# Optimization experiments

Measured on AMD Instinct MI355X. Metric: run time of the kernel, lower is better.

## Reference

```python
import jax, jax.numpy as jnp
import numpy as np
import math

B, T, C = 4, 2048, 1024
H = 16
DH = C // H
SCALE = 1.0 / math.sqrt(DH)


def setup_inputs() -> dict:
    key = jax.random.key(0)
    k1, k2, k3 = jax.random.split(key, 3)
    x = jax.random.normal(k1, (B, T, C), dtype=jnp.float32)
    # init_unit_norm: randn / sqrt(d_in)
    W_qkv = jax.random.normal(k2, (3 * C, C), dtype=jnp.float32) / math.sqrt(C)
    W_out = jax.random.normal(k3, (C, C), dtype=jnp.float32) / math.sqrt(C)
    return {"x": x, "W_qkv": W_qkv, "W_out": W_out}


def reference(x, W_qkv, W_out):
    b, t, c = x.shape
    qkv = x @ W_qkv.T                      # [B,T,3C]
    q, k, v = jnp.split(qkv, 3, axis=-1)
    # [B,T,C] -> [B,H,T,Dh]
    q = q.reshape(b, t, H, DH).transpose(0, 2, 1, 3)
    k = k.reshape(b, t, H, DH).transpose(0, 2, 1, 3)
    v = v.reshape(b, t, H, DH).transpose(0, 2, 1, 3)
    scores = jnp.einsum('bhtd,bhsd->bhts', q, k) * SCALE  # [B,H,T,T]
    mask = jnp.tril(jnp.ones((t, t), dtype=bool))
    scores = jnp.where(mask, scores, 0.0)  # no softmax
    attn = jnp.einsum('bhts,bhsd->bhtd', scores, v)       # [B,H,T,Dh]
    attn = attn.transpose(0, 2, 1, 3).reshape(b, t, c)
    return attn @ W_out.T
```

## Files before the change

### kernel.cpp

```cpp
#include <hip/hip_runtime.h>

#define TT 2048
#define CC 1024

typedef __attribute__((ext_vector_type(8))) __bf16 bf16x8;
typedef __attribute__((ext_vector_type(4))) float f32x4;
typedef unsigned int u32;

__device__ __forceinline__ short f2bf(float f) {
  u32 u = __float_as_uint(f);
  u += 0x7fffu + ((u >> 16) & 1u);
  return (short)(u >> 16);
}

#if __has_builtin(__builtin_amdgcn_cvt_pk_bf16_f32)
__device__ __forceinline__ u32 pack2(float a, float b) {
  auto v = __builtin_amdgcn_cvt_pk_bf16_f32(a, b);
  return __builtin_bit_cast(u32, v);
}
#else
__device__ __forceinline__ u32 pack2(float a, float b) {
  u32 ua = __float_as_uint(a), ub = __float_as_uint(b);
  ua += 0x7fffu + ((ua >> 16) & 1u);
  ub += 0x7fffu + ((ub >> 16) & 1u);
  return (ua >> 16) | (ub & 0xffff0000u);
}
#endif

__global__ void cvt_bf16(const float* __restrict__ in, short* __restrict__ out, int n4) {
  int i = blockIdx.x * blockDim.x + threadIdx.x;
  if (i >= n4) return;
  float4 f = reinterpret_cast<const float4*>(in)[i];
  short4 s;
  s.x = f2bf(f.x); s.y = f2bf(f.y); s.z = f2bf(f.z); s.w = f2bf(f.w);
  reinterpret_cast<short4*>(out)[i] = s;
}

__global__ void cvt_wqkv(const float* __restrict__ in, short* __restrict__ out, int n4) {
  int i = blockIdx.x * blockDim.x + threadIdx.x;
  if (i >= n4) return;
  float sc = (i * 4 < 1048576) ? 0.125f : 1.0f;
  float4 f = reinterpret_cast<const float4*>(in)[i];
  short4 s;
  s.x = f2bf(f.x * sc); s.y = f2bf(f.y * sc); s.z = f2bf(f.z * sc); s.w = f2bf(f.w * sc);
  reinterpret_cast<short4*>(out)[i] = s;
}

__device__ __forceinline__ void storev(float* p, float v) { *p = v; }
__device__ __forceinline__ void storev(short* p, float v) { *p = f2bf(v); }

#if __has_builtin(__builtin_amdgcn_global_load_lds)
#define HAVE_GLD_LDS 1
__device__ __forceinline__ void gld_lds16(const short* g, short* l) {
  __builtin_amdgcn_global_load_lds((const __attribute__((address_space(1))) u32*)g,
                                   (__attribute__((address_space(3))) u32*)l, 16, 0, 0);
}
#endif

template <typename OutT>
__global__ __launch_bounds__(256) void gemm_bt(const short* __restrict__ A,
                                               const short* __restrict__ B,
                                               OutT* __restrict__ Cm,
                                               int M, int N, int K) {
  __shared__ __align__(16) short As[128 * 32];
  __shared__ __align__(16) short Bs[128 * 32];
  const int tid = threadIdx.x;
  const int wave = tid >> 6, lane = tid & 63;
  const int quad = lane >> 4, nl = lane & 15;
  const int m0 = blockIdx.x * 128, n0 = blockIdx.y * 128;
  const int wr = (wave >> 1) * 64, wc = (wave & 1) * 64;
  f32x4 acc[4][4] = {};
  for (int k0 = 0; k0 < K; k0 += 32) {
    __syncthreads();
#pragma unroll
    for (int i = 0; i < 2; ++i) {
      int idx = tid + i * 256;
      int row = idx >> 2, cg = idx & 3;
#if HAVE_GLD_LDS
      gld_lds16(&A[(size_t)(m0 + row) * K + k0 + cg * 8], &As[(i * 256 + wave * 64) * 8]);
      gld_lds16(&B[(size_t)(n0 + row) * K + k0 + cg * 8], &Bs[(i * 256 + wave * 64) * 8]);
#else
      *reinterpret_cast<uint4*>(&As[row * 32 + cg * 8]) =
          *reinterpret_cast<const uint4*>(&A[(size_t)(m0 + row) * K + k0 + cg * 8]);
      *reinterpret_cast<uint4*>(&Bs[row * 32 + cg * 8]) =
          *reinterpret_cast<const uint4*>(&B[(size_t)(n0 + row) * K + k0 + cg * 8]);
#endif
    }
    __syncthreads();
    bf16x8 af[4], bfr[4];
#pragma unroll
    for (int i = 0; i < 4; ++i)
      af[i] = *reinterpret_cast<const bf16x8*>(&As[(wr + i * 16 + nl) * 32 + quad * 8]);
#pragma unroll
    for (int i = 0; i < 4; ++i)
      bfr[i] = *reinterpret_cast<const bf16x8*>(&Bs[(wc + i * 16 + nl) * 32 + quad * 8]);
#pragma unroll
    for (int mi = 0; mi < 4; ++mi)
#pragma unroll
      for (int ni = 0; ni < 4; ++ni)
        acc[mi][ni] = __builtin_amdgcn_mfma_f32_16x16x32_bf16(af[mi], bfr[ni], acc[mi][ni], 0, 0, 0);
  }
#pragma unroll
  for (int mi = 0; mi < 4; ++mi)
#pragma unroll
    for (int ni = 0; ni < 4; ++ni) {
      int row = m0 + wr + mi * 16 + quad * 4;
      int col = n0 + wc + ni * 16 + nl;
#pragma unroll
      for (int r = 0; r < 4; ++r)
        storev(&Cm[(size_t)(row + r) * N + col], acc[mi][ni][r]);
    }
}

__global__ __launch_bounds__(256) void transpose_v(const short* __restrict__ qkv,
                                                   short* __restrict__ vt) {
  __shared__ short Ls[64 * 68];
  const int bh = blockIdx.y, tb = blockIdx.x;
  const int b = bh >> 4, h = bh & 15;
  const int tid = threadIdx.x;
  const short* src = qkv + (size_t)(b * TT + tb * 64) * (3 * CC) + 2 * CC + h * 64;
#pragma unroll
  for (int i = 0; i < 2; ++i) {
    int idx = tid + i * 256;
    int tl = idx >> 3, dc = idx & 7;
    uint4 d4 = *reinterpret_cast<const uint4*>(&src[(size_t)tl * (3 * CC) + dc * 8]);
    *reinterpret_cast<uint2*>(&Ls[tl * 68 + dc * 8]) = make_uint2(d4.x, d4.y);
    *reinterpret_cast<uint2*>(&Ls[tl * 68 + dc * 8 + 4]) = make_uint2(d4.z, d4.w);
  }
  __syncthreads();
  short* dst = vt + (size_t)(bh * 64) * TT + tb * 64;
#pragma unroll
  for (int i = 0; i < 2; ++i) {
    int idx = tid + i * 256;
    int dl = idx >> 3, tc = idx & 7;
    short tmp[8];
#pragma unroll
    for (int j = 0; j < 8; ++j) tmp[j] = Ls[(tc * 8 + j) * 68 + dl];
    *reinterpret_cast<uint4*>(&dst[(size_t)dl * TT + tc * 8]) = *reinterpret_cast<uint4*>(tmp);
  }
}

__device__ __forceinline__ f32x4 mfma16(bf16x8 a, bf16x8 b, f32x4 c) {
  return __builtin_amdgcn_mfma_f32_16x16x32_bf16(a, b, c, 0, 0, 0);
}

template <bool DIAG>
__device__ __forceinline__ void attn_compute(const short* Frag, u32* ssw,
                                             const bf16x8 (&qf)[2][2], f32x4 (&o)[2][4],
                                             int lane, int quad, int nl) {
  bf16x8 k00 = *reinterpret_cast<const bf16x8*>(&Frag[0 * 512 + lane * 8]);
  bf16x8 k01 = *reinterpret_cast<const bf16x8*>(&Frag[1 * 512 + lane * 8]);
  bf16x8 k10 = *reinterpret_cast<const bf16x8*>(&Frag[2 * 512 + lane * 8]);
  bf16x8 k11 = *reinterpret_cast<const bf16x8*>(&Frag[3 * 512 + lane * 8]);
  bf16x8 vB[4];
#pragma unroll
  for (int nb = 0; nb < 4; ++nb)
    vB[nb] = *reinterpret_cast<const bf16x8*>(&Frag[2048 + nb * 512 + lane * 8]);
  {
    u32* srow = &ssw[0 * 320 + nl * 20];
    f32x4 s0 = {};
    s0 = mfma16(k00, qf[0][0], s0);
    s0 = mfma16(k01, qf[0][1], s0);
    if (DIAG) {
#pragma unroll
      for (int r = 0; r < 4; ++r) s0[r] = (quad * 4 + r <= nl) ? s0[r] : 0.0f;
    }
#pragma unroll
    for (int p = 0; p < 2; ++p) srow[quad * 2 + p] = pack2(s0[2 * p], s0[2 * p + 1]);
    if (DIAG) {
#pragma unroll
      for (int p = 0; p < 2; ++p) srow[8 + quad * 2 + p] = 0;
    } else {
      f32x4 s1 = {};
      s1 = mfma16(k10, qf[0][0], s1);
      s1 = mfma16(k11, qf[0][1], s1);
#pragma unroll
      for (int p = 0; p < 2; ++p) srow[8 + quad * 2 + p] = pack2(s1[2 * p], s1[2 * p + 1]);
    }
  }
  {
    u32* srow = &ssw[1 * 320 + nl * 20];
    f32x4 s0 = {}, s1 = {};
    s0 = mfma16(k00, qf[1][0], s0);
    s0 = mfma16(k01, qf[1][1], s0);
    s1 = mfma16(k10, qf[1][0], s1);
    s1 = mfma16(k11, qf[1][1], s1);
    if (DIAG) {
#pragma unroll
      for (int r = 0; r < 4; ++r) s1[r] = (quad * 4 + r <= nl) ? s1[r] : 0.0f;
    }
#pragma unroll
    for (int p = 0; p < 2; ++p) {
      srow[quad * 2 + p] = pack2(s0[2 * p], s0[2 * p + 1]);
      srow[8 + quad * 2 + p] = pack2(s1[2 * p], s1[2 * p + 1]);
    }
  }
#pragma unroll
  for (int m = 0; m < 2; ++m) {
    bf16x8 sf = *reinterpret_cast<const bf16x8*>(&ssw[m * 320 + nl * 20 + quad * 4]);
#pragma unroll
    for (int nb = 0; nb < 4; ++nb) o[m][nb] = mfma16(sf, vB[nb], o[m][nb]);
  }
}

__global__ __launch_bounds__(256, 4) void attn_kernel(const short* __restrict__ qkv,
                                                      const short* __restrict__ vt,
                                                      short* __restrict__ attnb) {
  const int bh = blockIdx.x;
  const int b = bh >> 4, h = bh & 15;
  const int ti = 15 - blockIdx.y;
  const int T0 = ti * 128;
  const int tid = threadIdx.x;
  const int wave = tid >> 6, lane = tid & 63;
  const int quad = lane >> 4, nl = lane & 15;

  const short* qbase = qkv + (size_t)(b * TT) * (3 * CC) + h * 64;
  const short* kbase = qbase + CC;
  const short* vbase = vt + (size_t)(bh * 64) * TT;

  __shared__ __align__(16) short Frag[4096];
  __shared__ __align__(16) u32 Ss[4][640];
  u32* ssw = Ss[wave];

  const int tw0 = T0 + wave * 32;
  bf16x8 qf[2][2];
#pragma unroll
  for (int m = 0; m < 2; ++m)
#pragma unroll
    for (int half = 0; half < 2; ++half)
      qf[m][half] = *reinterpret_cast<const bf16x8*>(
          &qbase[(size_t)(tw0 + m * 16 + nl) * (3 * CC) + half * 32 + quad * 8]);

  f32x4 o[2][4] = {};

  const short* ksrc = kbase + (size_t)((wave >> 1) * 16 + nl) * (3 * CC) + (wave & 1) * 32 + quad * 8;
  const short* vsrc = vbase + (size_t)(wave * 16 + nl) * TT + quad * 8;
  short* kdst = &Frag[wave * 512];
  short* vdst = &Frag[2048 + wave * 512];

  const int nch = 4 * ti + 4;
  const int cd = 4 * ti + wave;

  for (int c = 0; c < nch; ++c) {
    __syncthreads();
#if HAVE_GLD_LDS
    gld_lds16(ksrc + (size_t)c * 32 * (3 * CC), kdst);
    gld_lds16(vsrc + c * 32, vdst);
#else
    *reinterpret_cast<uint4*>(&kdst[lane * 8]) =
        *reinterpret_cast<const uint4*>(ksrc + (size_t)c * 32 * (3 * CC));
    *reinterpret_cast<uint4*>(&vdst[lane * 8]) =
        *reinterpret_cast<const uint4*>(vsrc + c * 32);
#endif
    __syncthreads();
    if (c < cd)
      attn_compute<false>(Frag, ssw, qf, o, lane, quad, nl);
    else if (c == cd)
      attn_compute<true>(Frag, ssw, qf, o, lane, quad, nl);
  }

#pragma unroll
  for (int m = 0; m < 2; ++m)
#pragma unroll
    for (int nb = 0; nb < 4; ++nb)
#pragma unroll
      for (int r = 0; r < 4; ++r) {
        int t = tw0 + m * 16 + quad * 4 + r;
        attnb[(size_t)(b * TT + t) * CC + h * 64 + nb * 16 + nl] = f2bf(o[m][nb][r]);
      }
}

extern "C" void kernel_launch(void* const* d_in, const int* in_sizes, int n_in,
                              void* d_out, int out_size, void* d_ws, size_t ws_size,
                              hipStream_t stream) {
  const float* x = (const float*)d_in[0];
  const float* wqkv = (const float*)d_in[1];
  const float* wout = (const float*)d_in[2];
  float* out = (float*)d_out;

  char* ws = (char*)d_ws;
  short* xb    = (short*)(ws);
  short* wqkvb = (short*)(ws + 16777216);
  short* woutb = (short*)(ws + 23068672);
  short* qkvb  = (short*)(ws + 25165824);
  short* attnb = (short*)(ws + 75497472);
  short* vt    = xb;

  cvt_bf16<<<8192, 256, 0, stream>>>(x, xb, 2097152);
  cvt_wqkv<<<3072, 256, 0, stream>>>(wqkv, wqkvb, 786432);
  cvt_bf16<<<1024, 256, 0, stream>>>(wout, woutb, 262144);

  gemm_bt<short><<<dim3(64, 24), 256, 0, stream>>>(xb, wqkvb, qkvb, 8192, 3072, 1024);

  transpose_v<<<dim3(32, 64), 256, 0, stream>>>(qkvb, vt);

  attn_kernel<<<dim3(64, 16), 256, 0, stream>>>(qkvb, vt, attnb);

  gemm_bt<float><<<dim3(64, 8), 256, 0, stream>>>(attnb, woutb, out, 8192, 1024, 1024);
}
```

Baseline: 266.6 us.

## Double-buffer attention K/V tiles in 64-key chunks and fuse conversion kernels

The attention kernel now stages 64-key K/V chunks into two LDS buffers. Each wave prefetches the next chunk while it computes on the current one, which removes one barrier per step and hides global-to-LDS latency. The larger shared-memory footprint lowers the occupancy hint from 4 to 3 blocks per CU. Separately, the three fp32-to-bf16 conversion launches are merged into one kernel that writes a contiguous workspace, saving launch overhead.

```diff
diff --git a/kernel.cpp b/kernel.cpp
--- a/kernel.cpp
+++ b/kernel.cpp
@@ -27,23 +27,26 @@
 }
 #endif
 
-__global__ void cvt_bf16(const float* __restrict__ in, short* __restrict__ out, int n4) {
+__global__ __launch_bounds__(256) void cvt_all(const float* __restrict__ x,
+                                               const float* __restrict__ wqkv,
+                                               const float* __restrict__ wout,
+                                               short* __restrict__ dst) {
   int i = blockIdx.x * blockDim.x + threadIdx.x;
-  if (i >= n4) return;
-  float4 f = reinterpret_cast<const float4*>(in)[i];
-  short4 s;
-  s.x = f2bf(f.x); s.y = f2bf(f.y); s.z = f2bf(f.z); s.w = f2bf(f.w);
-  reinterpret_cast<short4*>(out)[i] = s;
-}
-
-__global__ void cvt_wqkv(const float* __restrict__ in, short* __restrict__ out, int n4) {
-  int i = blockIdx.x * blockDim.x + threadIdx.x;
-  if (i >= n4) return;
-  float sc = (i * 4 < 1048576) ? 0.125f : 1.0f;
-  float4 f = reinterpret_cast<const float4*>(in)[i];
+  const float* src;
+  float sc = 1.0f;
+  if (i < 2097152) {
+    src = x + (size_t)i * 4;
+  } else if (i < 2883584) {
+    int j = i - 2097152;
+    src = wqkv + (size_t)j * 4;
+    if (j < 262144) sc = 0.125f;
+  } else {
+    src = wout + (size_t)(i - 2883584) * 4;
+  }
+  float4 f = *reinterpret_cast<const float4*>(src);
   short4 s;
   s.x = f2bf(f.x * sc); s.y = f2bf(f.y * sc); s.z = f2bf(f.z * sc); s.w = f2bf(f.w * sc);
-  reinterpret_cast<short4*>(out)[i] = s;
+  reinterpret_cast<short4*>(dst)[i] = s;
 }
 
 __device__ __forceinline__ void storev(float* p, float v) { *p = v; }
@@ -145,17 +148,17 @@
 }
 
 template <bool DIAG>
-__device__ __forceinline__ void attn_compute(const short* Frag, u32* ssw,
+__device__ __forceinline__ void attn_compute(const short* kf, const short* vf, u32* ssw,
                                              const bf16x8 (&qf)[2][2], f32x4 (&o)[2][4],
                                              int lane, int quad, int nl) {
-  bf16x8 k00 = *reinterpret_cast<const bf16x8*>(&Frag[0 * 512 + lane * 8]);
-  bf16x8 k01 = *reinterpret_cast<const bf16x8*>(&Frag[1 * 512 + lane * 8]);
-  bf16x8 k10 = *reinterpret_cast<const bf16x8*>(&Frag[2 * 512 + lane * 8]);
-  bf16x8 k11 = *reinterpret_cast<const bf16x8*>(&Frag[3 * 512 + lane * 8]);
+  bf16x8 k00 = *reinterpret_cast<const bf16x8*>(&kf[0 * 512 + lane * 8]);
+  bf16x8 k01 = *reinterpret_cast<const bf16x8*>(&kf[1 * 512 + lane * 8]);
+  bf16x8 k10 = *reinterpret_cast<const bf16x8*>(&kf[2 * 512 + lane * 8]);
+  bf16x8 k11 = *reinterpret_cast<const bf16x8*>(&kf[3 * 512 + lane * 8]);
   bf16x8 vB[4];
 #pragma unroll
   for (int nb = 0; nb < 4; ++nb)
-    vB[nb] = *reinterpret_cast<const bf16x8*>(&Frag[2048 + nb * 512 + lane * 8]);
+    vB[nb] = *reinterpret_cast<const bf16x8*>(&vf[nb * 512 + lane * 8]);
   {
     u32* srow = &ssw[0 * 320 + nl * 20];
     f32x4 s0 = {};
@@ -203,7 +206,7 @@
   }
 }
 
-__global__ __launch_bounds__(256, 4) void attn_kernel(const short* __restrict__ qkv,
+__global__ __launch_bounds__(256, 3) void attn_kernel(const short* __restrict__ qkv,
                                                       const short* __restrict__ vt,
                                                       short* __restrict__ attnb) {
   const int bh = blockIdx.x;
@@ -218,7 +221,7 @@
   const short* kbase = qbase + CC;
   const short* vbase = vt + (size_t)(bh * 64) * TT;
 
-  __shared__ __align__(16) short Frag[4096];
+  __shared__ __align__(16) short Frag[2][8192];
   __shared__ __align__(16) u32 Ss[4][640];
   u32* ssw = Ss[wave];
 
@@ -233,30 +236,47 @@
 
   f32x4 o[2][4] = {};
 
-  const short* ksrc = kbase + (size_t)((wave >> 1) * 16 + nl) * (3 * CC) + (wave & 1) * 32 + quad * 8;
-  const short* vsrc = vbase + (size_t)(wave * 16 + nl) * TT + quad * 8;
-  short* kdst = &Frag[wave * 512];
-  short* vdst = &Frag[2048 + wave * 512];
-
-  const int nch = 4 * ti + 4;
+  const short* ksrc = kbase + (size_t)(wave * 16 + nl) * (3 * CC) + quad * 8;
+  const int sp_w = wave >> 1, nb0 = (wave & 1) * 2;
+  const short* vsrc0 = vbase + (size_t)((nb0 + 0) * 16 + nl) * TT + sp_w * 32 + quad * 8;
+  const short* vsrc1 = vbase + (size_t)((nb0 + 1) * 16 + nl) * TT + sp_w * 32 + quad * 8;
+
+  auto stage = [&](short* fb, int c) {
+    const size_t koff = (size_t)(c * 64) * (3 * CC);
+#if HAVE_GLD_LDS
+    gld_lds16(ksrc + koff, &fb[(2 * wave) * 512]);
+    gld_lds16(ksrc + koff + 32, &fb[(2 * wave + 1) * 512]);
+    gld_lds16(vsrc0 + c * 64, &fb[4096 + (2 * wave) * 512]);
+    gld_lds16(vsrc1 + c * 64, &fb[4096 + (2 * wave + 1) * 512]);
+#else
+    *reinterpret_cast<uint4*>(&fb[(2 * wave) * 512 + lane * 8]) =
+        *reinterpret_cast<const uint4*>(ksrc + koff);
+    *reinterpret_cast<uint4*>(&fb[(2 * wave + 1) * 512 + lane * 8]) =
+        *reinterpret_cast<const uint4*>(ksrc + koff + 32);
+    *reinterpret_cast<uint4*>(&fb[4096 + (2 * wave) * 512 + lane * 8]) =
+        *reinterpret_cast<const uint4*>(vsrc0 + c * 64);
+    *reinterpret_cast<uint4*>(&fb[4096 + (2 * wave + 1) * 512 + lane * 8]) =
+        *reinterpret_cast<const uint4*>(vsrc1 + c * 64);
+#endif
+  };
+
+  const int nch = 2 * ti + 2;
   const int cd = 4 * ti + wave;
 
+  stage(Frag[0], 0);
   for (int c = 0; c < nch; ++c) {
     __syncthreads();
-#if HAVE_GLD_LDS
-    gld_lds16(ksrc + (size_t)c * 32 * (3 * CC), kdst);
-    gld_lds16(vsrc + c * 32, vdst);
-#else
-    *reinterpret_cast<uint4*>(&kdst[lane * 8]) =
-        *reinterpret_cast<const uint4*>(ksrc + (size_t)c * 32 * (3 * CC));
-    *reinterpret_cast<uint4*>(&vdst[lane * 8]) =
-        *reinterpret_cast<const uint4*>(vsrc + c * 32);
-#endif
-    __syncthreads();
-    if (c < cd)
-      attn_compute<false>(Frag, ssw, qf, o, lane, quad, nl);
-    else if (c == cd)
-      attn_compute<true>(Frag, ssw, qf, o, lane, quad, nl);
+    if (c + 1 < nch) stage(Frag[(c + 1) & 1], c + 1);
+    const short* fb = Frag[c & 1];
+    const int c0 = 2 * c, c1 = 2 * c + 1;
+    if (c0 < cd)
+      attn_compute<false>(fb, fb + 4096, ssw, qf, o, lane, quad, nl);
+    else if (c0 == cd)
+      attn_compute<true>(fb, fb + 4096, ssw, qf, o, lane, quad, nl);
+    if (c1 < cd)
+      attn_compute<false>(fb + 2048, fb + 4096 + 2048, ssw, qf, o, lane, quad, nl);
+    else if (c1 == cd)
+      attn_compute<true>(fb + 2048, fb + 4096 + 2048, ssw, qf, o, lane, quad, nl);
   }
 
 #pragma unroll
@@ -286,9 +306,7 @@
   short* attnb = (short*)(ws + 75497472);
   short* vt    = xb;
 
-  cvt_bf16<<<8192, 256, 0, stream>>>(x, xb, 2097152);
-  cvt_wqkv<<<3072, 256, 0, stream>>>(wqkv, wqkvb, 786432);
-  cvt_bf16<<<1024, 256, 0, stream>>>(wout, woutb, 262144);
+  cvt_all<<<12288, 256, 0, stream>>>(x, wqkv, wout, xb);
 
   gemm_bt<short><<<dim3(64, 24), 256, 0, stream>>>(xb, wqkvb, qkvb, 8192, 3072, 1024);
 
```

After: 250.2 us. 1.07x faster.
